# Optimization experiments

Hardware: AMD Instinct MI355X
Metric: run time of the kernel (lower is better)

## Reference

```python
import jax, jax.numpy as jnp
import numpy as np

B, LK, D, H = 16, 4096, 1024, 16
DK = D // H
EPS = 1e-5
NEG = -1.0e9


def _layernorm(x, g, b):
    m = jnp.mean(x, axis=-1, keepdims=True)
    v = jnp.mean((x - m) ** 2, axis=-1, keepdims=True)
    return (x - m) * jax.lax.rsqrt(v + EPS) * g + b


def setup_inputs() -> dict:
    key0 = jax.random.key(0)
    ks = jax.random.split(key0, 12)

    def lin(k, fan_in, fan_out):
        # torch nn.Linear default-ish scale; stored as [in, out] so y = x @ W + b
        return jax.random.normal(k, (fan_in, fan_out), jnp.float32) / np.float32(np.sqrt(fan_in))

    return {
        "query": jax.random.normal(ks[0], (B, 1, D), jnp.float32),
        "key": jax.random.normal(ks[1], (B, LK, D), jnp.float32),
        "mask": jax.random.randint(ks[2], (B, 1, LK), 0, 2, jnp.int32),
        "Wq": lin(ks[3], D, D), "bq": jnp.zeros((D,), jnp.float32),
        "Wk": lin(ks[4], D, D), "bk": jnp.zeros((D,), jnp.float32),
        "Wv": lin(ks[5], D, D), "bv": jnp.zeros((D,), jnp.float32),
        "Wo": lin(ks[6], D, D), "bo": jnp.zeros((D,), jnp.float32),
        "raw_thr": jnp.full((H, 1, 1), 0.1, jnp.float32),
        "Wvp": lin(ks[7], 2 * D, D),  # v_proj, no bias
        "W1": lin(ks[8], D, 2 * D), "b1": jnp.zeros((2 * D,), jnp.float32),
        "W2": lin(ks[9], 2 * D, D), "b2": jnp.zeros((D,), jnp.float32),
        "g1": jnp.ones((D,), jnp.float32), "be1": jnp.zeros((D,), jnp.float32),
        "g2": jnp.ones((D,), jnp.float32), "be2": jnp.zeros((D,), jnp.float32),
    }


def reference(query, key, mask, Wq, bq, Wk, bk, Wv, bv, Wo, bo, raw_thr,
              Wvp, W1, b1, W2, b2, g1, be1, g2, be2):
    b = query.shape[0]
    lk = key.shape[1]
    # v = cat(key, query.repeat(1, Lk, 1)) @ Wvp   (query has seq_len 1)
    v_in = jnp.concatenate([key, jnp.broadcast_to(query, (b, lk, D))], axis=2)
    v = v_in @ Wvp  # [B, Lk, D]

    Q = (query @ Wq + bq).reshape(b, 1, H, DK).transpose(0, 2, 1, 3)   # [B,H,1,DK]
    K = (key @ Wk + bk).reshape(b, lk, H, DK).transpose(0, 2, 1, 3)    # [B,H,Lk,DK]
    V = (v @ Wv + bv).reshape(b, lk, H, DK).transpose(0, 2, 1, 3)      # [B,H,Lk,DK]

    scores = jnp.einsum("bhqd,bhkd->bhqk", Q, K) / jnp.sqrt(jnp.float32(DK))
    # padding mask: [B,1,Lk] -> [B,1,1,Lk]
    scores = jnp.where(mask[:, None] == 0, NEG, scores)
    # learned per-head threshold: softplus(raw_thr) -> [1,H,1,1]
    thr = jax.nn.softplus(raw_thr)[None]
    scores = jnp.where(scores <= thr, NEG, scores)
    attn = jax.nn.softmax(scores, axis=-1)

    x = jnp.einsum("bhqk,bhkd->bhqd", attn, V)            # [B,H,1,DK]
    x = x.transpose(0, 2, 1, 3).reshape(b, 1, H * DK)      # [B,1,D]
    attn_out = x @ Wo + bo

    x = _layernorm(query + attn_out, g1, be1)
    ff = jax.nn.relu(x @ W1 + b1) @ W2 + b2
    x = _layernorm(x + ff, g2, be2)
    return x
```

## Files before the change

### kernel.cpp

```cpp
#include <hip/hip_runtime.h>
#include <hip/hip_bf16.h>

#define NB 16
#define NHD 16
#define ND 1024
#define NLK 4096
#define NFF 2048

typedef float f32x4 __attribute__((ext_vector_type(4)));
typedef float f32x2 __attribute__((ext_vector_type(2)));
typedef __bf16 bf16x2v __attribute__((ext_vector_type(2)));
typedef __bf16 bf16x4v __attribute__((ext_vector_type(4)));
typedef __bf16 bf16x8 __attribute__((ext_vector_type(8)));

__global__ void k_fill(float* out, int n, float v) {
  int i = blockIdx.x * 256 + threadIdx.x;
  if (i < n) out[i] = v;
}

__device__ __forceinline__ void gbar(unsigned* ctr, unsigned* flg, unsigned nblk) {
  __syncthreads();
  if (threadIdx.x == 0) {
    __hip_atomic_fetch_add(ctr, 1u, __ATOMIC_RELEASE, __HIP_MEMORY_SCOPE_AGENT);
    if (blockIdx.x == 0) {
      while (__hip_atomic_load(ctr, __ATOMIC_RELAXED, __HIP_MEMORY_SCOPE_AGENT) < nblk)
        __builtin_amdgcn_s_sleep(8);
      __hip_atomic_store(flg, 1u, __ATOMIC_RELEASE, __HIP_MEMORY_SCOPE_AGENT);
    } else {
      while (__hip_atomic_load(flg, __ATOMIC_RELAXED, __HIP_MEMORY_SCOPE_AGENT) == 0)
        __builtin_amdgcn_s_sleep(8);
    }
    __builtin_amdgcn_fence(__ATOMIC_ACQUIRE, "agent");
  }
  __syncthreads();
}

__global__ __launch_bounds__(256) void k_pre(const float* __restrict__ Wq,
                                             const float* __restrict__ bq,
                                             const float* __restrict__ Wvp,
                                             const float* __restrict__ query,
                                             const float* __restrict__ Wk,
                                             const float* __restrict__ bk,
                                             float* __restrict__ Qrow,
                                             float* __restrict__ cvec,
                                             __hip_bfloat16* __restrict__ wvpt,
                                             __hip_bfloat16* __restrict__ t_bf,
                                             float* __restrict__ s0,
                                             unsigned* __restrict__ bar) {
  __shared__ float pmem[9472];
  int blk = blockIdx.x;
  int t = threadIdx.x;
  if (blk < 128) {
    int which = blk >> 6;
    int jb = blk & 3;
    int i0 = ((blk >> 2) & 15) * 64;
    int j = jb * 256 + t;
    {
      int e = t * 4;
      int b = e >> 6, ii = e & 63;
      float4 v = *(const float4*)(query + (size_t)b * ND + i0 + ii);
      pmem[ii * 20 + b] = v.x;
      pmem[(ii + 1) * 20 + b] = v.y;
      pmem[(ii + 2) * 20 + b] = v.z;
      pmem[(ii + 3) * 20 + b] = v.w;
    }
    __syncthreads();
    float acc[16];
#pragma unroll
    for (int q = 0; q < 16; ++q) acc[q] = 0.f;
    for (int ii = 0; ii < 64; ++ii) {
      int i = i0 + ii;
      float wv = which ? Wvp[(size_t)(ND + i) * ND + j] : Wq[(size_t)i * ND + j];
      float qv[16];
      const float4* qp = (const float4*)&pmem[ii * 20];
      *(float4*)&qv[0] = qp[0];
      *(float4*)&qv[4] = qp[1];
      *(float4*)&qv[8] = qp[2];
      *(float4*)&qv[12] = qp[3];
#pragma unroll
      for (int q = 0; q < 16; ++q) acc[q] += wv * qv[q];
    }
    float* out = which ? cvec : Qrow;
    float bias = (!which && i0 == 0) ? bq[j] : 0.f;
#pragma unroll
    for (int q = 0; q < 16; ++q) atomicAdd(&out[q * ND + j], acc[q] + bias);
  } else {
    int tb = blk - 128;
    int n0 = (tb & 15) * 64;
    int k0base = (tb >> 4) * 256;
    for (int it = 0; it < 4; ++it) {
      int k0 = k0base + it * 64;
#pragma unroll
      for (int i = 0; i < 4; ++i) {
        int idx = t * 4 + i * 1024;
        int kk = idx >> 6, nn = idx & 63;
        float4 v = *(const float4*)(Wvp + (size_t)(k0 + kk) * ND + n0 + nn);
        pmem[kk * 68 + nn] = v.x;
        pmem[kk * 68 + nn + 1] = v.y;
        pmem[kk * 68 + nn + 2] = v.z;
        pmem[kk * 68 + nn + 3] = v.w;
      }
      __syncthreads();
#pragma unroll
      for (int i = 0; i < 4; ++i) {
        int idx = t * 4 + i * 1024;
        int nn = idx >> 6, kk = idx & 63;
        bf16x4v o;
#pragma unroll
        for (int j = 0; j < 4; ++j) o[j] = (__bf16)pmem[(kk + j) * 68 + nn];
        *(bf16x4v*)((__bf16*)wvpt + (size_t)(n0 + nn) * ND + k0 + kk) = o;
      }
      __syncthreads();
    }
  }
  gbar(&bar[5 * 32], &bar[256 + 5 * 32], 192);
  {
    int h = blk & 15, dblk = blk >> 4;
    float* qs = pmem;
    float* wks = pmem + 1024;
    if (blk < 128) {
      int lin = t * 4;
      int bb = lin >> 6, dk = lin & 63;
      *(float4*)&qs[bb * 64 + dk] = *(const float4*)(Qrow + bb * ND + h * 64 + dk);
#pragma unroll
      for (int e = 0; e < 8; ++e) {
        int l2 = e * 1024 + t * 4;
        int d = l2 >> 6, dk2 = l2 & 63;
        *(float4*)&wks[d * 66 + dk2] =
            *(const float4*)(Wk + (size_t)(dblk * 128 + d) * ND + h * 64 + dk2);
      }
    }
    __syncthreads();
    if (blk < 128) {
      if (dblk == 0 && t < 16) {
        float a = 0.f;
        const float* bkh = bk + h * 64;
        for (int jj = 0; jj < 64; ++jj) a += bkh[jj] * qs[t * 64 + jj];
        s0[t * 16 + h] = a;
      }
      int d = t >> 1, bh = (t & 1) * 8;
      float acc[8];
#pragma unroll
      for (int q = 0; q < 8; ++q) acc[q] = 0.f;
      for (int dk = 0; dk < 64; ++dk) {
        float wv = wks[d * 66 + dk];
#pragma unroll
        for (int q = 0; q < 8; ++q) acc[q] += wv * qs[(bh + q) * 64 + dk];
      }
#pragma unroll
      for (int q = 0; q < 8; ++q)
        t_bf[(size_t)((bh + q) * 16 + h) * ND + dblk * 128 + d] = (__hip_bfloat16)acc[q];
    }
  }
}

__global__ __launch_bounds__(512, 4) void k_flash(const float* __restrict__ key,
                                                  const __hip_bfloat16* __restrict__ t_bf,
                                                  const float* __restrict__ s0,
                                                  const float* __restrict__ raw_thr,
                                                  const int* __restrict__ mask,
                                                  __hip_bfloat16* __restrict__ pu,
                                                  float* __restrict__ mloc,
                                                  float* __restrict__ lloc) {
  int ch = blockIdx.x, b = blockIdx.y;
  int t = threadIdx.x;
  int wv = t >> 6, lane = t & 63, l15 = lane & 15, g4 = lane >> 4;
  __shared__ __align__(16) unsigned char lds_arena[79360];
  __bf16* kstage = (__bf16*)lds_arena;
  __bf16* psb = (__bf16*)(lds_arena + 65536);
  float* scr = (float*)(lds_arena + 74752);
  float* wls = (float*)(lds_arena + 76928);
  float* sm = (float*)(lds_arena + 78976);
  float* mrun = sm;
  float* lrun = sm + 16;
  float* fact = sm + 32;
  float* mnewv = sm + 48;
  float* thv = sm + 64;
  float* s0v = sm + 80;

  f32x2 pu_r[16];
#pragma unroll
  for (int h = 0; h < 16; ++h) pu_r[h] = (f32x2){0.f, 0.f};
  if (t < 16) {
    mrun[t] = -1.0e9f;
    lrun[t] = 0.f;
    thv[t] = log1pf(expf(raw_thr[t]));
    s0v[t] = s0[b * 16 + t];
  }
  __syncthreads();
  const float* keyb = key + (size_t)b * NLK * ND;
  const __hip_bfloat16* tb = t_bf + (size_t)(b * 16 + l15) * ND;
  int dsl = wv * 128;
  __bf16* kst_w = kstage + wv * 4096;
  int kk = t >> 4, hh = t & 15;
  int c16 = lane >> 2, bofs = (lane & 3) * 2;
  for (int sp = 0; sp < 4; ++sp) {
    int ks0 = ch * 128 + sp * 32;
    f32x4 sa0 = {0.f, 0.f, 0.f, 0.f}, sa1 = {0.f, 0.f, 0.f, 0.f};
#pragma unroll
    for (int st = 0; st < 4; ++st) {
      int d = dsl + st * 32 + g4 * 8;
      bf16x8 bfr = *(const bf16x8*)(tb + d);
      const float* a0p = keyb + (size_t)(ks0 + l15) * ND + d;
      const float* a1p = a0p + (size_t)16 * ND;
      float a0[8], a1[8];
      *(float4*)&a0[0] = *(const float4*)a0p;
      *(float4*)&a0[4] = *(const float4*)(a0p + 4);
      *(float4*)&a1[0] = *(const float4*)a1p;
      *(float4*)&a1[4] = *(const float4*)(a1p + 4);
      bf16x8 af0, af1;
#pragma unroll
      for (int j = 0; j < 8; ++j) {
        af0[j] = (__bf16)a0[j];
        af1[j] = (__bf16)a1[j];
      }
      int pos = (((st * 4 + g4) ^ l15) & 15) * 8;
      *(bf16x8*)(kst_w + l15 * 128 + pos) = af0;
      *(bf16x8*)(kst_w + (16 + l15) * 128 + pos) = af1;
      sa0 = __builtin_amdgcn_mfma_f32_16x16x32_bf16(af0, bfr, sa0, 0, 0, 0);
      sa1 = __builtin_amdgcn_mfma_f32_16x16x32_bf16(af1, bfr, sa1, 0, 0, 0);
    }
#pragma unroll
    for (int r = 0; r < 4; ++r) {
      psb[(wv * 32 + g4 * 4 + r) * 18 + l15] = (__bf16)sa0[r];
      psb[(wv * 32 + 16 + g4 * 4 + r) * 18 + l15] = (__bf16)sa1[r];
    }
    __syncthreads();
    float sum = 0.f;
#pragma unroll
    for (int w = 0; w < 8; ++w) sum += (float)psb[(w * 32 + kk) * 18 + hh];
    float sc_ = (sum + s0v[hh]) * 0.125f;
    int mv = mask[b * NLK + ks0 + kk];
    float sv = (mv != 0 && sc_ > thv[hh]) ? sc_ : -1.0e9f;
    scr[kk * 17 + hh] = sv;
    __syncthreads();
    if (wv == 0) {
      float m = -3.4e38f;
#pragma unroll
      for (int j = 0; j < 8; ++j) m = fmaxf(m, scr[(g4 * 8 + j) * 17 + l15]);
      m = fmaxf(m, __shfl_xor(m, 16, 64));
      m = fmaxf(m, __shfl_xor(m, 32, 64));
      if (lane < 16) {
        float mn = fmaxf(mrun[lane], m);
        mnewv[lane] = mn;
        fact[lane] = expf(mrun[lane] - mn);
        mrun[lane] = mn;
      }
    }
    __syncthreads();
    float w = expf(sv - mnewv[hh]);
    scr[kk * 17 + hh] = w;
    wls[kk * 16 + hh] = w;
    __syncthreads();
    if (wv == 0) {
      float s = 0.f;
#pragma unroll
      for (int j = 0; j < 8; ++j) s += scr[(g4 * 8 + j) * 17 + l15];
      s += __shfl_xor(s, 16, 64);
      s += __shfl_xor(s, 32, 64);
      if (lane < 16) lrun[lane] = lrun[lane] * fact[lane] + s;
    }
#pragma unroll
    for (int h = 0; h < 16; ++h) pu_r[h] *= fact[h];
    for (int k = 0; k < 32; ++k) {
      int phys = ((c16 ^ k) & 15) * 8;
      unsigned u = *(const unsigned*)(kst_w + k * 128 + phys + bofs);
      f32x2 kv;
      kv[0] = __uint_as_float(u << 16);
      kv[1] = __uint_as_float(u & 0xffff0000u);
      const f32x4* wr = (const f32x4*)&wls[k * 16];
      f32x4 w0 = wr[0], w1 = wr[1], w2 = wr[2], w3 = wr[3];
#pragma unroll
      for (int q = 0; q < 4; ++q) {
        pu_r[q] += w0[q] * kv;
        pu_r[4 + q] += w1[q] * kv;
        pu_r[8 + q] += w2[q] * kv;
        pu_r[12 + q] += w3[q] * kv;
      }
    }
  }
  int dlane = dsl + lane * 2;
  size_t pubase = (size_t)((b * 32 + ch) * 16) * ND + dlane;
#pragma unroll
  for (int h = 0; h < 16; ++h) {
    bf16x2v o;
    o[0] = (__bf16)pu_r[h][0];
    o[1] = (__bf16)pu_r[h][1];
    *(bf16x2v*)((__bf16*)pu + pubase + (size_t)h * ND) = o;
  }
  if (t < 16) {
    mloc[(b * 32 + ch) * 16 + t] = mrun[t];
    lloc[(b * 32 + ch) * 16 + t] = lrun[t];
  }
}

__global__ __launch_bounds__(256, 2) void k_tail(
    const __hip_bfloat16* __restrict__ pu, const float* __restrict__ mloc,
    const float* __restrict__ lloc, __hip_bfloat16* __restrict__ u_bf,
    const __hip_bfloat16* __restrict__ wvpt,
    const float* __restrict__ cvec, const float* __restrict__ Wv,
    const float* __restrict__ bv, float* __restrict__ attn_x,
    const float* __restrict__ Wo, const float* __restrict__ bo,
    const float* __restrict__ query, float* __restrict__ r1,
    const float* __restrict__ g1, const float* __restrict__ be1,
    const float* __restrict__ W1, float* __restrict__ h1,
    const float* __restrict__ b1, const float* __restrict__ W2,
    float* __restrict__ out2, const float* __restrict__ b2,
    const float* __restrict__ g2, const float* __restrict__ be2,
    float* __restrict__ outp, unsigned* __restrict__ bar) {
  __shared__ float smf[2176];
  int blk = blockIdx.x, t = threadIdx.x;
  int wv = t >> 6, lane = t & 63, l15 = lane & 15, g4 = lane >> 4;

  {
    int g = blk * 256 + t;
    if (g < 16384) {
      attn_x[g] = 0.f;
      r1[g] = 0.f;
      out2[g] = 0.f;
    }
    if (g < 32768) h1[g] = 0.f;
    int b = blk >> 4, h = blk & 15;
    if (t < 32) {
      float m = mloc[(b * 32 + t) * 16 + h];
      float l = lloc[(b * 32 + t) * 16 + h];
      float mg = m;
      for (int o = 16; o > 0; o >>= 1) mg = fmaxf(mg, __shfl_xor(mg, o, 32));
      float term = l * expf(m - mg);
      float ls = term;
      for (int o = 16; o > 0; o >>= 1) ls += __shfl_xor(ls, o, 32);
      smf[t] = expf(m - mg) / ls;
    }
    __syncthreads();
    int d = t * 4;
    f32x4 acc = {0.f, 0.f, 0.f, 0.f};
    for (int c = 0; c < 32; ++c) {
      bf16x4v v4 = *(const bf16x4v*)((const __bf16*)pu +
                                     (size_t)((b * 32 + c) * 16 + h) * ND + d);
      f32x4 v = {(float)v4[0], (float)v4[1], (float)v4[2], (float)v4[3]};
      acc += smf[c] * v;
    }
    bf16x4v o;
#pragma unroll
    for (int j = 0; j < 4; ++j) o[j] = (__bf16)acc[j];
    *(bf16x4v*)((__bf16*)u_bf + (size_t)(b * 16 + h) * ND + d) = o;
  }
  gbar(&bar[0 * 32], &bar[256 + 0 * 32], 256);

  {
    int h = blk >> 4, d0 = (blk & 15) * 64;
    float* vb = smf;
    const __hip_bfloat16* ub = u_bf + (size_t)(l15 * 16 + h) * ND;
    const __hip_bfloat16* wb = wvpt + (size_t)(d0 + wv * 16 + l15) * ND;
    f32x4 acc = {0.f, 0.f, 0.f, 0.f};
    for (int ks = 0; ks < 32; ++ks) {
      int d = ks * 32 + g4 * 8;
      bf16x8 a = *(const bf16x8*)(ub + d);
      bf16x8 bb = *(const bf16x8*)(wb + d);
      acc = __builtin_amdgcn_mfma_f32_16x16x32_bf16(a, bb, acc, 0, 0, 0);
    }
#pragma unroll
    for (int r = 0; r < 4; ++r) {
      int b = g4 * 4 + r;
      int nn = wv * 16 + l15;
      vb[b * 68 + nn] = acc[r] + cvec[(size_t)b * ND + d0 + nn];
    }
    __syncthreads();
    int joff = t & 63, bg = t >> 6;
    int j = h * 64 + joff;
    float ax[4] = {0.f, 0.f, 0.f, 0.f};
    for (int dd = 0; dd < 64; ++dd) {
      float wv_ = Wv[(size_t)(d0 + dd) * ND + j];
#pragma unroll
      for (int q = 0; q < 4; ++q) ax[q] += wv_ * vb[(bg * 4 + q) * 68 + dd];
    }
#pragma unroll
    for (int q = 0; q < 4; ++q) {
      float val = ax[q];
      if ((blk & 15) == 0) val += bv[j];
      atomicAdd(&attn_x[(size_t)(bg * 4 + q) * ND + j], val);
    }
  }
  gbar(&bar[1 * 32], &bar[256 + 1 * 32], 256);

  {
    int j0 = (blk & 7) * 128;
    int dc = blk >> 3;
    int d0 = dc * 32;
    float* ax = smf;
    if (t < 128) {
      int lin = t * 4;
      int bb = lin >> 5, dd = lin & 31;
      *(float4*)&ax[bb * 36 + dd] = *(const float4*)(attn_x + (size_t)bb * ND + d0 + dd);
    }
    __syncthreads();
    int joff = t & 127, bg = t >> 7;
    int j = j0 + joff;
    float acc[8];
#pragma unroll
    for (int q = 0; q < 8; ++q) acc[q] = 0.f;
    for (int dd = 0; dd < 32; ++dd) {
      float wv_ = Wo[(size_t)(d0 + dd) * ND + j];
#pragma unroll
      for (int q = 0; q < 8; ++q) acc[q] += wv_ * ax[(bg * 8 + q) * 36 + dd];
    }
#pragma unroll
    for (int q = 0; q < 8; ++q) {
      int bb = bg * 8 + q;
      float val = acc[q];
      if (dc == 0) val += bo[j] + query[(size_t)bb * ND + j];
      atomicAdd(&r1[(size_t)bb * ND + j], val);
    }
  }
  gbar(&bar[2 * 32], &bar[256 + 2 * 32], 256);

  {
    int n = (blk & 7) * 256 + t;
    int d0 = (blk >> 3) * 32;
    float* xs = smf;
    float* mv_s = smf + 1984;
    float* iv_s = smf + 2000;
    {
      int row = t >> 4, seg = t & 15;
      float s = 0.f, s2 = 0.f;
      const float* rp = r1 + (size_t)row * ND + seg * 64;
      for (int q = 0; q < 16; ++q) {
        float4 v = *(const float4*)(rp + q * 4);
        s += v.x + v.y + v.z + v.w;
        s2 += v.x * v.x + v.y * v.y + v.z * v.z + v.w * v.w;
      }
      for (int o = 1; o < 16; o <<= 1) {
        s += __shfl_xor(s, o, 16);
        s2 += __shfl_xor(s2, o, 16);
      }
      if (seg == 0) {
        float mean = s * (1.f / ND);
        float var = s2 * (1.f / ND) - mean * mean;
        mv_s[row] = mean;
        iv_s[row] = rsqrtf(var + 1e-5f);
      }
    }
    __syncthreads();
    if (t < 128) {
      int e = t * 4;
      int bb = e >> 5, dd = e & 31;
      float4 v = *(const float4*)(r1 + (size_t)bb * ND + d0 + dd);
      float4 g = *(const float4*)(g1 + d0 + dd);
      float4 be = *(const float4*)(be1 + d0 + dd);
      float m = mv_s[bb], iv = iv_s[bb];
      xs[bb * 36 + dd] = (v.x - m) * iv * g.x + be.x;
      xs[bb * 36 + dd + 1] = (v.y - m) * iv * g.y + be.y;
      xs[bb * 36 + dd + 2] = (v.z - m) * iv * g.z + be.z;
      xs[bb * 36 + dd + 3] = (v.w - m) * iv * g.w + be.w;
    }
    __syncthreads();
    float acc[16];
#pragma unroll
    for (int q = 0; q < 16; ++q) acc[q] = 0.f;
    for (int dd = 0; dd < 32; ++dd) {
      float wv_ = W1[(size_t)(d0 + dd) * NFF + n];
#pragma unroll
      for (int q = 0; q < 16; ++q) acc[q] += wv_ * xs[q * 36 + dd];
    }
#pragma unroll
    for (int q = 0; q < 16; ++q) atomicAdd(&h1[(size_t)q * NFF + n], acc[q]);
  }
  gbar(&bar[3 * 32], &bar[256 + 3 * 32], 256);

  {
    int j0 = (blk & 7) * 128;
    int n0 = (blk >> 3) * 64;
    float* hs = smf;
    {
      int lin = t * 4;
      int bb = lin >> 6, nn = lin & 63;
      float4 hv = *(const float4*)(h1 + (size_t)bb * NFF + n0 + nn);
      float4 bb1 = *(const float4*)(b1 + n0 + nn);
      hs[bb * 68 + nn] = fmaxf(hv.x + bb1.x, 0.f);
      hs[bb * 68 + nn + 1] = fmaxf(hv.y + bb1.y, 0.f);
      hs[bb * 68 + nn + 2] = fmaxf(hv.z + bb1.z, 0.f);
      hs[bb * 68 + nn + 3] = fmaxf(hv.w + bb1.w, 0.f);
    }
    __syncthreads();
    int joff = t & 127, bg = t >> 7;
    int j = j0 + joff;
    float acc[8];
#pragma unroll
    for (int q = 0; q < 8; ++q) acc[q] = 0.f;
    for (int nn = 0; nn < 64; ++nn) {
      float wv_ = W2[(size_t)(n0 + nn) * ND + j];
#pragma unroll
      for (int q = 0; q < 8; ++q) acc[q] += wv_ * hs[(bg * 8 + q) * 68 + nn];
    }
#pragma unroll
    for (int q = 0; q < 8; ++q) atomicAdd(&out2[(size_t)(bg * 8 + q) * ND + j], acc[q]);
  }
  gbar(&bar[4 * 32], &bar[256 + 4 * 32], 256);

  if (blk < 16) {
    int b = blk;
    float* rs = smf;
    float* rs2 = smf + 256;
    float4 v = *(const float4*)(r1 + (size_t)b * ND + t * 4);
    float s = v.x + v.y + v.z + v.w;
    float s2 = v.x * v.x + v.y * v.y + v.z * v.z + v.w * v.w;
    rs[t] = s;
    rs2[t] = s2;
    __syncthreads();
    for (int st = 128; st > 0; st >>= 1) {
      if (t < st) {
        rs[t] += rs[t + st];
        rs2[t] += rs2[t + st];
      }
      __syncthreads();
    }
    float mean = rs[0] * (1.f / ND);
    float var = rs2[0] * (1.f / ND) - mean * mean;
    float inv = rsqrtf(var + 1e-5f);
    float4 g = *(const float4*)(g1 + t * 4);
    float4 be = *(const float4*)(be1 + t * 4);
    float4 o2 = *(const float4*)(out2 + (size_t)b * ND + t * 4);
    float4 bb2 = *(const float4*)(b2 + t * 4);
    float4 v2;
    v2.x = (v.x - mean) * inv * g.x + be.x + o2.x + bb2.x;
    v2.y = (v.y - mean) * inv * g.y + be.y + o2.y + bb2.y;
    v2.z = (v.z - mean) * inv * g.z + be.z + o2.z + bb2.z;
    v2.w = (v.w - mean) * inv * g.w + be.w + o2.w + bb2.w;
    __syncthreads();
    s = v2.x + v2.y + v2.z + v2.w;
    s2 = v2.x * v2.x + v2.y * v2.y + v2.z * v2.z + v2.w * v2.w;
    rs[t] = s;
    rs2[t] = s2;
    __syncthreads();
    for (int st = 128; st > 0; st >>= 1) {
      if (t < st) {
        rs[t] += rs[t + st];
        rs2[t] += rs2[t + st];
      }
      __syncthreads();
    }
    float mean2 = rs[0] * (1.f / ND);
    float var2 = rs2[0] * (1.f / ND) - mean2 * mean2;
    float inv2 = rsqrtf(var2 + 1e-5f);
    float4 gg = *(const float4*)(g2 + t * 4);
    float4 bbe = *(const float4*)(be2 + t * 4);
    float4 o;
    o.x = (v2.x - mean2) * inv2 * gg.x + bbe.x;
    o.y = (v2.y - mean2) * inv2 * gg.y + bbe.y;
    o.z = (v2.z - mean2) * inv2 * gg.z + bbe.z;
    o.w = (v2.w - mean2) * inv2 * gg.w + bbe.w;
    *(float4*)(outp + (size_t)b * ND + t * 4) = o;
  }
}

extern "C" void kernel_launch(void* const* d_in, const int* in_sizes, int n_in,
                              void* d_out, int out_size, void* d_ws, size_t ws_size,
                              hipStream_t stream) {
  const float* query = (const float*)d_in[0];
  const float* key = (const float*)d_in[1];
  const int* mask = (const int*)d_in[2];
  const float* Wq = (const float*)d_in[3];
  const float* bq = (const float*)d_in[4];
  const float* Wk = (const float*)d_in[5];
  const float* bk = (const float*)d_in[6];
  const float* Wv = (const float*)d_in[7];
  const float* bv = (const float*)d_in[8];
  const float* Wo = (const float*)d_in[9];
  const float* bo = (const float*)d_in[10];
  const float* raw_thr = (const float*)d_in[11];
  const float* Wvp = (const float*)d_in[12];
  const float* W1 = (const float*)d_in[13];
  const float* b1 = (const float*)d_in[14];
  const float* W2 = (const float*)d_in[15];
  const float* b2 = (const float*)d_in[16];
  const float* g1 = (const float*)d_in[17];
  const float* be1 = (const float*)d_in[18];
  const float* g2 = (const float*)d_in[19];
  const float* be2 = (const float*)d_in[20];

  const size_t OFF_QROW = 0;
  const size_t OFF_C = 65536;
  const size_t OFF_BAR = 131072;
  const size_t ZERO_BYTES = 135168;
  const size_t OFF_ATTNX = 135168;
  const size_t OFF_R1 = 200704;
  const size_t OFF_H1 = 266240;
  const size_t OFF_OUT2 = 397312;
  const size_t OFF_S0 = 462848;
  const size_t OFF_MLOC = 463872;
  const size_t OFF_LLOC = 496640;
  const size_t OFF_TBF = 529408;
  const size_t OFF_UBF = 1053696;
  const size_t OFF_WVPT = 1577984;
  const size_t OFF_PU = 4723712;
  const size_t TOTAL = 21500928;

  if (ws_size < TOTAL) {
    k_fill<<<dim3((out_size + 255) / 256), dim3(256), 0, stream>>>((float*)d_out, out_size,
                                                                   12345.0f);
    return;
  }

  char* wsb = (char*)d_ws;
  float* Qrow = (float*)(wsb + OFF_QROW);
  float* cvec = (float*)(wsb + OFF_C);
  unsigned* bar = (unsigned*)(wsb + OFF_BAR);
  float* attn_x = (float*)(wsb + OFF_ATTNX);
  float* r1 = (float*)(wsb + OFF_R1);
  float* h1 = (float*)(wsb + OFF_H1);
  float* out2 = (float*)(wsb + OFF_OUT2);
  float* s0 = (float*)(wsb + OFF_S0);
  float* mloc = (float*)(wsb + OFF_MLOC);
  float* lloc = (float*)(wsb + OFF_LLOC);
  __hip_bfloat16* t_bf = (__hip_bfloat16*)(wsb + OFF_TBF);
  __hip_bfloat16* u_bf = (__hip_bfloat16*)(wsb + OFF_UBF);
  __hip_bfloat16* wvpt = (__hip_bfloat16*)(wsb + OFF_WVPT);
  __hip_bfloat16* pu = (__hip_bfloat16*)(wsb + OFF_PU);

  hipMemsetAsync(d_ws, 0, ZERO_BYTES, stream);

  k_pre<<<dim3(192), dim3(256), 0, stream>>>(Wq, bq, Wvp, query, Wk, bk, Qrow, cvec, wvpt,
                                             t_bf, s0, bar);
  k_flash<<<dim3(32, 16), dim3(512), 0, stream>>>(key, t_bf, s0, raw_thr, mask, pu, mloc, lloc);
  k_tail<<<dim3(256), dim3(256), 0, stream>>>(pu, mloc, lloc, u_bf, wvpt, cvec, Wv, bv,
                                              attn_x, Wo, bo, query, r1, g1, be1, W1, h1, b1,
                                              W2, out2, b2, g2, be2, (float*)d_out, bar);
}
```

Before: 192.3 us.

## Fuse prologue kernel into flash kernel using grid-wide barriers

Merges the k_pre prologue (Q/cvec projections, Wvp transpose, t_bf precompute) into the k_flash kernel as a 512-block persistent launch separated by two software grid barriers. The prologue work is repartitioned for 512-thread blocks. The aim is to drop one kernel launch and the inter-kernel gap. In exchange, all 512 blocks must be co-resident for the barriers to work, and most blocks sit idle through the prologue phases. The barrier flag offsets in k_tail are shifted to match the new layout.

```diff
diff --git a/kernel.cpp b/kernel.cpp
--- a/kernel.cpp
+++ b/kernel.cpp
@@ -35,262 +35,258 @@
   __syncthreads();
 }
 
-__global__ __launch_bounds__(256) void k_pre(const float* __restrict__ Wq,
-                                             const float* __restrict__ bq,
-                                             const float* __restrict__ Wvp,
-                                             const float* __restrict__ query,
-                                             const float* __restrict__ Wk,
-                                             const float* __restrict__ bk,
-                                             float* __restrict__ Qrow,
-                                             float* __restrict__ cvec,
-                                             __hip_bfloat16* __restrict__ wvpt,
-                                             __hip_bfloat16* __restrict__ t_bf,
-                                             float* __restrict__ s0,
-                                             unsigned* __restrict__ bar) {
-  __shared__ float pmem[9472];
-  int blk = blockIdx.x;
-  int t = threadIdx.x;
+__global__ __launch_bounds__(512, 4) void k_flash(
+    const float* __restrict__ Wq, const float* __restrict__ bq,
+    const float* __restrict__ Wvp, const float* __restrict__ query,
+    const float* __restrict__ Wk, const float* __restrict__ bk,
+    float* __restrict__ Qrow, float* __restrict__ cvec,
+    __hip_bfloat16* __restrict__ wvpt, __hip_bfloat16* __restrict__ t_bf,
+    float* __restrict__ s0,
+    const float* __restrict__ key, const float* __restrict__ raw_thr,
+    const int* __restrict__ mask, __hip_bfloat16* __restrict__ pu,
+    float* __restrict__ mloc, float* __restrict__ lloc,
+    unsigned* __restrict__ bar) {
+  __shared__ __align__(16) unsigned char lds_arena[79360];
+  float* af = (float*)lds_arena;
+  int blk = blockIdx.x, t = threadIdx.x;
+  int wv = t >> 6, lane = t & 63, l15 = lane & 15, g4 = lane >> 4;
+  int half = t >> 8, vt = t & 255;
+
   if (blk < 128) {
     int which = blk >> 6;
-    int jb = blk & 3;
-    int i0 = ((blk >> 2) & 15) * 64;
-    int j = jb * 256 + t;
-    {
+    int jb = (blk >> 5) & 1;
+    int i0c = blk & 31;
+    int i0 = i0c * 32;
+    int j = jb * 512 + t;
+    if (t < 128) {
       int e = t * 4;
-      int b = e >> 6, ii = e & 63;
+      int b = e >> 5, ii = e & 31;
       float4 v = *(const float4*)(query + (size_t)b * ND + i0 + ii);
-      pmem[ii * 20 + b] = v.x;
-      pmem[(ii + 1) * 20 + b] = v.y;
-      pmem[(ii + 2) * 20 + b] = v.z;
-      pmem[(ii + 3) * 20 + b] = v.w;
+      af[ii * 20 + b] = v.x;
+      af[(ii + 1) * 20 + b] = v.y;
+      af[(ii + 2) * 20 + b] = v.z;
+      af[(ii + 3) * 20 + b] = v.w;
     }
     __syncthreads();
     float acc[16];
 #pragma unroll
     for (int q = 0; q < 16; ++q) acc[q] = 0.f;
-    for (int ii = 0; ii < 64; ++ii) {
+    for (int ii = 0; ii < 32; ++ii) {
       int i = i0 + ii;
-      float wv = which ? Wvp[(size_t)(ND + i) * ND + j] : Wq[(size_t)i * ND + j];
+      float wvv = which ? Wvp[(size_t)(ND + i) * ND + j] : Wq[(size_t)i * ND + j];
       float qv[16];
-      const float4* qp = (const float4*)&pmem[ii * 20];
+      const float4* qp = (const float4*)&af[ii * 20];
       *(float4*)&qv[0] = qp[0];
       *(float4*)&qv[4] = qp[1];
       *(float4*)&qv[8] = qp[2];
       *(float4*)&qv[12] = qp[3];
 #pragma unroll
-      for (int q = 0; q < 16; ++q) acc[q] += wv * qv[q];
+      for (int q = 0; q < 16; ++q) acc[q] += wvv * qv[q];
     }
     float* out = which ? cvec : Qrow;
-    float bias = (!which && i0 == 0) ? bq[j] : 0.f;
+    float bias = (!which && i0c == 0) ? bq[j] : 0.f;
 #pragma unroll
     for (int q = 0; q < 16; ++q) atomicAdd(&out[q * ND + j], acc[q] + bias);
-  } else {
+  } else if (blk < 192) {
     int tb = blk - 128;
     int n0 = (tb & 15) * 64;
     int k0base = (tb >> 4) * 256;
     for (int it = 0; it < 4; ++it) {
       int k0 = k0base + it * 64;
 #pragma unroll
-      for (int i = 0; i < 4; ++i) {
-        int idx = t * 4 + i * 1024;
+      for (int i = 0; i < 2; ++i) {
+        int idx = t * 4 + i * 2048;
         int kk = idx >> 6, nn = idx & 63;
         float4 v = *(const float4*)(Wvp + (size_t)(k0 + kk) * ND + n0 + nn);
-        pmem[kk * 68 + nn] = v.x;
-        pmem[kk * 68 + nn + 1] = v.y;
-        pmem[kk * 68 + nn + 2] = v.z;
-        pmem[kk * 68 + nn + 3] = v.w;
-      }
-      __syncthreads();
-#pragma unroll
-      for (int i = 0; i < 4; ++i) {
-        int idx = t * 4 + i * 1024;
+        af[kk * 68 + nn] = v.x;
+        af[kk * 68 + nn + 1] = v.y;
+        af[kk * 68 + nn + 2] = v.z;
+        af[kk * 68 + nn + 3] = v.w;
+      }
+      __syncthreads();
+#pragma unroll
+      for (int i = 0; i < 2; ++i) {
+        int idx = t * 4 + i * 2048;
         int nn = idx >> 6, kk = idx & 63;
         bf16x4v o;
 #pragma unroll
-        for (int j = 0; j < 4; ++j) o[j] = (__bf16)pmem[(kk + j) * 68 + nn];
+        for (int jj = 0; jj < 4; ++jj) o[jj] = (__bf16)af[(kk + jj) * 68 + nn];
         *(bf16x4v*)((__bf16*)wvpt + (size_t)(n0 + nn) * ND + k0 + kk) = o;
       }
       __syncthreads();
     }
   }
-  gbar(&bar[5 * 32], &bar[256 + 5 * 32], 192);
-  {
-    int h = blk & 15, dblk = blk >> 4;
-    float* qs = pmem;
-    float* wks = pmem + 1024;
-    if (blk < 128) {
-      int lin = t * 4;
+  gbar(&bar[6 * 32], &bar[512 + 6 * 32], 512);
+
+  if (blk < 64) {
+    int h = blk & 15;
+    int dblk = (blk >> 4) * 2 + half;
+    float* pm = af + half * 9472;
+    float* qs = pm;
+    float* wks = pm + 1024;
+    {
+      int lin = vt * 4;
       int bb = lin >> 6, dk = lin & 63;
       *(float4*)&qs[bb * 64 + dk] = *(const float4*)(Qrow + bb * ND + h * 64 + dk);
-#pragma unroll
-      for (int e = 0; e < 8; ++e) {
-        int l2 = e * 1024 + t * 4;
-        int d = l2 >> 6, dk2 = l2 & 63;
-        *(float4*)&wks[d * 66 + dk2] =
-            *(const float4*)(Wk + (size_t)(dblk * 128 + d) * ND + h * 64 + dk2);
-      }
-    }
-    __syncthreads();
-    if (blk < 128) {
-      if (dblk == 0 && t < 16) {
-        float a = 0.f;
-        const float* bkh = bk + h * 64;
-        for (int jj = 0; jj < 64; ++jj) a += bkh[jj] * qs[t * 64 + jj];
-        s0[t * 16 + h] = a;
-      }
-      int d = t >> 1, bh = (t & 1) * 8;
-      float acc[8];
-#pragma unroll
-      for (int q = 0; q < 8; ++q) acc[q] = 0.f;
-      for (int dk = 0; dk < 64; ++dk) {
-        float wv = wks[d * 66 + dk];
-#pragma unroll
-        for (int q = 0; q < 8; ++q) acc[q] += wv * qs[(bh + q) * 64 + dk];
-      }
-#pragma unroll
-      for (int q = 0; q < 8; ++q)
-        t_bf[(size_t)((bh + q) * 16 + h) * ND + dblk * 128 + d] = (__hip_bfloat16)acc[q];
-    }
-  }
-}
-
-__global__ __launch_bounds__(512, 4) void k_flash(const float* __restrict__ key,
-                                                  const __hip_bfloat16* __restrict__ t_bf,
-                                                  const float* __restrict__ s0,
-                                                  const float* __restrict__ raw_thr,
-                                                  const int* __restrict__ mask,
-                                                  __hip_bfloat16* __restrict__ pu,
-                                                  float* __restrict__ mloc,
-                                                  float* __restrict__ lloc) {
-  int ch = blockIdx.x, b = blockIdx.y;
-  int t = threadIdx.x;
-  int wv = t >> 6, lane = t & 63, l15 = lane & 15, g4 = lane >> 4;
-  __shared__ __align__(16) unsigned char lds_arena[79360];
-  __bf16* kstage = (__bf16*)lds_arena;
-  __bf16* psb = (__bf16*)(lds_arena + 65536);
-  float* scr = (float*)(lds_arena + 74752);
-  float* wls = (float*)(lds_arena + 76928);
-  float* sm = (float*)(lds_arena + 78976);
-  float* mrun = sm;
-  float* lrun = sm + 16;
-  float* fact = sm + 32;
-  float* mnewv = sm + 48;
-  float* thv = sm + 64;
-  float* s0v = sm + 80;
-
-  f32x2 pu_r[16];
-#pragma unroll
-  for (int h = 0; h < 16; ++h) pu_r[h] = (f32x2){0.f, 0.f};
-  if (t < 16) {
-    mrun[t] = -1.0e9f;
-    lrun[t] = 0.f;
-    thv[t] = log1pf(expf(raw_thr[t]));
-    s0v[t] = s0[b * 16 + t];
-  }
-  __syncthreads();
-  const float* keyb = key + (size_t)b * NLK * ND;
-  const __hip_bfloat16* tb = t_bf + (size_t)(b * 16 + l15) * ND;
-  int dsl = wv * 128;
-  __bf16* kst_w = kstage + wv * 4096;
-  int kk = t >> 4, hh = t & 15;
-  int c16 = lane >> 2, bofs = (lane & 3) * 2;
-  for (int sp = 0; sp < 4; ++sp) {
-    int ks0 = ch * 128 + sp * 32;
-    f32x4 sa0 = {0.f, 0.f, 0.f, 0.f}, sa1 = {0.f, 0.f, 0.f, 0.f};
-#pragma unroll
-    for (int st = 0; st < 4; ++st) {
-      int d = dsl + st * 32 + g4 * 8;
-      bf16x8 bfr = *(const bf16x8*)(tb + d);
-      const float* a0p = keyb + (size_t)(ks0 + l15) * ND + d;
-      const float* a1p = a0p + (size_t)16 * ND;
-      float a0[8], a1[8];
-      *(float4*)&a0[0] = *(const float4*)a0p;
-      *(float4*)&a0[4] = *(const float4*)(a0p + 4);
-      *(float4*)&a1[0] = *(const float4*)a1p;
-      *(float4*)&a1[4] = *(const float4*)(a1p + 4);
-      bf16x8 af0, af1;
-#pragma unroll
-      for (int j = 0; j < 8; ++j) {
-        af0[j] = (__bf16)a0[j];
-        af1[j] = (__bf16)a1[j];
-      }
-      int pos = (((st * 4 + g4) ^ l15) & 15) * 8;
-      *(bf16x8*)(kst_w + l15 * 128 + pos) = af0;
-      *(bf16x8*)(kst_w + (16 + l15) * 128 + pos) = af1;
-      sa0 = __builtin_amdgcn_mfma_f32_16x16x32_bf16(af0, bfr, sa0, 0, 0, 0);
-      sa1 = __builtin_amdgcn_mfma_f32_16x16x32_bf16(af1, bfr, sa1, 0, 0, 0);
-    }
-#pragma unroll
-    for (int r = 0; r < 4; ++r) {
-      psb[(wv * 32 + g4 * 4 + r) * 18 + l15] = (__bf16)sa0[r];
-      psb[(wv * 32 + 16 + g4 * 4 + r) * 18 + l15] = (__bf16)sa1[r];
-    }
-    __syncthreads();
-    float sum = 0.f;
-#pragma unroll
-    for (int w = 0; w < 8; ++w) sum += (float)psb[(w * 32 + kk) * 18 + hh];
-    float sc_ = (sum + s0v[hh]) * 0.125f;
-    int mv = mask[b * NLK + ks0 + kk];
-    float sv = (mv != 0 && sc_ > thv[hh]) ? sc_ : -1.0e9f;
-    scr[kk * 17 + hh] = sv;
-    __syncthreads();
-    if (wv == 0) {
-      float m = -3.4e38f;
-#pragma unroll
-      for (int j = 0; j < 8; ++j) m = fmaxf(m, scr[(g4 * 8 + j) * 17 + l15]);
-      m = fmaxf(m, __shfl_xor(m, 16, 64));
-      m = fmaxf(m, __shfl_xor(m, 32, 64));
-      if (lane < 16) {
-        float mn = fmaxf(mrun[lane], m);
-        mnewv[lane] = mn;
-        fact[lane] = expf(mrun[lane] - mn);
-        mrun[lane] = mn;
-      }
-    }
-    __syncthreads();
-    float w = expf(sv - mnewv[hh]);
-    scr[kk * 17 + hh] = w;
-    wls[kk * 16 + hh] = w;
-    __syncthreads();
-    if (wv == 0) {
-      float s = 0.f;
-#pragma unroll
-      for (int j = 0; j < 8; ++j) s += scr[(g4 * 8 + j) * 17 + l15];
-      s += __shfl_xor(s, 16, 64);
-      s += __shfl_xor(s, 32, 64);
-      if (lane < 16) lrun[lane] = lrun[lane] * fact[lane] + s;
-    }
-#pragma unroll
-    for (int h = 0; h < 16; ++h) pu_r[h] *= fact[h];
-    for (int k = 0; k < 32; ++k) {
-      int phys = ((c16 ^ k) & 15) * 8;
-      unsigned u = *(const unsigned*)(kst_w + k * 128 + phys + bofs);
-      f32x2 kv;
-      kv[0] = __uint_as_float(u << 16);
-      kv[1] = __uint_as_float(u & 0xffff0000u);
-      const f32x4* wr = (const f32x4*)&wls[k * 16];
-      f32x4 w0 = wr[0], w1 = wr[1], w2 = wr[2], w3 = wr[3];
-#pragma unroll
-      for (int q = 0; q < 4; ++q) {
-        pu_r[q] += w0[q] * kv;
-        pu_r[4 + q] += w1[q] * kv;
-        pu_r[8 + q] += w2[q] * kv;
-        pu_r[12 + q] += w3[q] * kv;
-      }
-    }
-  }
-  int dlane = dsl + lane * 2;
-  size_t pubase = (size_t)((b * 32 + ch) * 16) * ND + dlane;
-#pragma unroll
-  for (int h = 0; h < 16; ++h) {
-    bf16x2v o;
-    o[0] = (__bf16)pu_r[h][0];
-    o[1] = (__bf16)pu_r[h][1];
-    *(bf16x2v*)((__bf16*)pu + pubase + (size_t)h * ND) = o;
-  }
-  if (t < 16) {
-    mloc[(b * 32 + ch) * 16 + t] = mrun[t];
-    lloc[(b * 32 + ch) * 16 + t] = lrun[t];
+    }
+#pragma unroll
+    for (int e = 0; e < 8; ++e) {
+      int l2 = e * 1024 + vt * 4;
+      int d = l2 >> 6, dk2 = l2 & 63;
+      *(float4*)&wks[d * 66 + dk2] =
+          *(const float4*)(Wk + (size_t)(dblk * 128 + d) * ND + h * 64 + dk2);
+    }
+    __syncthreads();
+    if (dblk == 0 && vt < 16) {
+      float a = 0.f;
+      const float* bkh = bk + h * 64;
+      for (int jj = 0; jj < 64; ++jj) a += bkh[jj] * qs[vt * 64 + jj];
+      s0[vt * 16 + h] = a;
+    }
+    int d = vt >> 1, bh = (vt & 1) * 8;
+    float acc[8];
+#pragma unroll
+    for (int q = 0; q < 8; ++q) acc[q] = 0.f;
+    for (int dk = 0; dk < 64; ++dk) {
+      float wvv = wks[d * 66 + dk];
+#pragma unroll
+      for (int q = 0; q < 8; ++q) acc[q] += wvv * qs[(bh + q) * 64 + dk];
+    }
+#pragma unroll
+    for (int q = 0; q < 8; ++q)
+      t_bf[(size_t)((bh + q) * 16 + h) * ND + dblk * 128 + d] = (__hip_bfloat16)acc[q];
+  }
+  gbar(&bar[7 * 32], &bar[512 + 7 * 32], 512);
+
+  {
+    int ch = blk & 31, b = blk >> 5;
+    __bf16* kstage = (__bf16*)lds_arena;
+    __bf16* psb = (__bf16*)(lds_arena + 65536);
+    float* scr = (float*)(lds_arena + 74752);
+    float* wls = (float*)(lds_arena + 76928);
+    float* sm = (float*)(lds_arena + 78976);
+    float* mrun = sm;
+    float* lrun = sm + 16;
+    float* fact = sm + 32;
+    float* mnewv = sm + 48;
+    float* thv = sm + 64;
+    float* s0v = sm + 80;
+
+    f32x2 pu_r[16];
+#pragma unroll
+    for (int h = 0; h < 16; ++h) pu_r[h] = (f32x2){0.f, 0.f};
+    __syncthreads();
+    if (t < 16) {
+      mrun[t] = -1.0e9f;
+      lrun[t] = 0.f;
+      thv[t] = log1pf(expf(raw_thr[t]));
+      s0v[t] = s0[b * 16 + t];
+    }
+    __syncthreads();
+    const float* keyb = key + (size_t)b * NLK * ND;
+    const __hip_bfloat16* tb = t_bf + (size_t)(b * 16 + l15) * ND;
+    int dsl = wv * 128;
+    __bf16* kst_w = kstage + wv * 4096;
+    int kk = t >> 4, hh = t & 15;
+    int c16 = lane >> 2, bofs = (lane & 3) * 2;
+    for (int sp = 0; sp < 4; ++sp) {
+      int ks0 = ch * 128 + sp * 32;
+      f32x4 sa0 = {0.f, 0.f, 0.f, 0.f}, sa1 = {0.f, 0.f, 0.f, 0.f};
+#pragma unroll
+      for (int st = 0; st < 4; ++st) {
+        int d = dsl + st * 32 + g4 * 8;
+        bf16x8 bfr = *(const bf16x8*)(tb + d);
+        const float* a0p = keyb + (size_t)(ks0 + l15) * ND + d;
+        const float* a1p = a0p + (size_t)16 * ND;
+        float a0[8], a1[8];
+        *(float4*)&a0[0] = *(const float4*)a0p;
+        *(float4*)&a0[4] = *(const float4*)(a0p + 4);
+        *(float4*)&a1[0] = *(const float4*)a1p;
+        *(float4*)&a1[4] = *(const float4*)(a1p + 4);
+        bf16x8 af0, af1;
+#pragma unroll
+        for (int j = 0; j < 8; ++j) {
+          af0[j] = (__bf16)a0[j];
+          af1[j] = (__bf16)a1[j];
+        }
+        int pos = (((st * 4 + g4) ^ l15) & 15) * 8;
+        *(bf16x8*)(kst_w + l15 * 128 + pos) = af0;
+        *(bf16x8*)(kst_w + (16 + l15) * 128 + pos) = af1;
+        sa0 = __builtin_amdgcn_mfma_f32_16x16x32_bf16(af0, bfr, sa0, 0, 0, 0);
+        sa1 = __builtin_amdgcn_mfma_f32_16x16x32_bf16(af1, bfr, sa1, 0, 0, 0);
+      }
+#pragma unroll
+      for (int r = 0; r < 4; ++r) {
+        psb[(wv * 32 + g4 * 4 + r) * 18 + l15] = (__bf16)sa0[r];
+        psb[(wv * 32 + 16 + g4 * 4 + r) * 18 + l15] = (__bf16)sa1[r];
+      }
+      __syncthreads();
+      float sum = 0.f;
+#pragma unroll
+      for (int w = 0; w < 8; ++w) sum += (float)psb[(w * 32 + kk) * 18 + hh];
+      float sc_ = (sum + s0v[hh]) * 0.125f;
+      int mv = mask[b * NLK + ks0 + kk];
+      float sv = (mv != 0 && sc_ > thv[hh]) ? sc_ : -1.0e9f;
+      scr[kk * 17 + hh] = sv;
+      __syncthreads();
+      if (wv == 0) {
+        float m = -3.4e38f;
+#pragma unroll
+        for (int j = 0; j < 8; ++j) m = fmaxf(m, scr[(g4 * 8 + j) * 17 + l15]);
+        m = fmaxf(m, __shfl_xor(m, 16, 64));
+        m = fmaxf(m, __shfl_xor(m, 32, 64));
+        if (lane < 16) {
+          float mn = fmaxf(mrun[lane], m);
+          mnewv[lane] = mn;
+          fact[lane] = expf(mrun[lane] - mn);
+          mrun[lane] = mn;
+        }
+      }
+      __syncthreads();
+      float w = expf(sv - mnewv[hh]);
+      scr[kk * 17 + hh] = w;
+      wls[kk * 16 + hh] = w;
+      __syncthreads();
+      if (wv == 0) {
+        float s = 0.f;
+#pragma unroll
+        for (int j = 0; j < 8; ++j) s += scr[(g4 * 8 + j) * 17 + l15];
+        s += __shfl_xor(s, 16, 64);
+        s += __shfl_xor(s, 32, 64);
+        if (lane < 16) lrun[lane] = lrun[lane] * fact[lane] + s;
+      }
+#pragma unroll
+      for (int h = 0; h < 16; ++h) pu_r[h] *= fact[h];
+      for (int k = 0; k < 32; ++k) {
+        int phys = ((c16 ^ k) & 15) * 8;
+        unsigned u = *(const unsigned*)(kst_w + k * 128 + phys + bofs);
+        f32x2 kv;
+        kv[0] = __uint_as_float(u << 16);
+        kv[1] = __uint_as_float(u & 0xffff0000u);
+        const f32x4* wr = (const f32x4*)&wls[k * 16];
+        f32x4 w0 = wr[0], w1 = wr[1], w2 = wr[2], w3 = wr[3];
+#pragma unroll
+        for (int q = 0; q < 4; ++q) {
+          pu_r[q] += w0[q] * kv;
+          pu_r[4 + q] += w1[q] * kv;
+          pu_r[8 + q] += w2[q] * kv;
+          pu_r[12 + q] += w3[q] * kv;
+        }
+      }
+    }
+    int dlane = dsl + lane * 2;
+    size_t pubase = (size_t)((b * 32 + ch) * 16) * ND + dlane;
+#pragma unroll
+    for (int h = 0; h < 16; ++h) {
+      bf16x2v o;
+      o[0] = (__bf16)pu_r[h][0];
+      o[1] = (__bf16)pu_r[h][1];
+      *(bf16x2v*)((__bf16*)pu + pubase + (size_t)h * ND) = o;
+    }
+    if (t < 16) {
+      mloc[(b * 32 + ch) * 16 + t] = mrun[t];
+      lloc[(b * 32 + ch) * 16 + t] = lrun[t];
+    }
   }
 }
 
@@ -345,7 +341,7 @@
     for (int j = 0; j < 4; ++j) o[j] = (__bf16)acc[j];
     *(bf16x4v*)((__bf16*)u_bf + (size_t)(b * 16 + h) * ND + d) = o;
   }
-  gbar(&bar[0 * 32], &bar[256 + 0 * 32], 256);
+  gbar(&bar[0 * 32], &bar[512 + 0 * 32], 256);
 
   {
     int h = blk >> 4, d0 = (blk & 15) * 64;
@@ -381,7 +377,7 @@
       atomicAdd(&attn_x[(size_t)(bg * 4 + q) * ND + j], val);
     }
   }
-  gbar(&bar[1 * 32], &bar[256 + 1 * 32], 256);
+  gbar(&bar[1 * 32], &bar[512 + 1 * 32], 256);
 
   {
     int j0 = (blk & 7) * 128;
@@ -412,7 +408,7 @@
       atomicAdd(&r1[(size_t)bb * ND + j], val);
     }
   }
-  gbar(&bar[2 * 32], &bar[256 + 2 * 32], 256);
+  gbar(&bar[2 * 32], &bar[512 + 2 * 32], 256);
 
   {
     int n = (blk & 7) * 256 + t;
@@ -465,7 +461,7 @@
 #pragma unroll
     for (int q = 0; q < 16; ++q) atomicAdd(&h1[(size_t)q * NFF + n], acc[q]);
   }
-  gbar(&bar[3 * 32], &bar[256 + 3 * 32], 256);
+  gbar(&bar[3 * 32], &bar[512 + 3 * 32], 256);
 
   {
     int j0 = (blk & 7) * 128;
@@ -495,7 +491,7 @@
 #pragma unroll
     for (int q = 0; q < 8; ++q) atomicAdd(&out2[(size_t)(bg * 8 + q) * ND + j], acc[q]);
   }
-  gbar(&bar[4 * 32], &bar[256 + 4 * 32], 256);
+  gbar(&bar[4 * 32], &bar[512 + 4 * 32], 256);
 
   if (blk < 16) {
     int b = blk;
@@ -619,9 +615,9 @@
 
   hipMemsetAsync(d_ws, 0, ZERO_BYTES, stream);
 
-  k_pre<<<dim3(192), dim3(256), 0, stream>>>(Wq, bq, Wvp, query, Wk, bk, Qrow, cvec, wvpt,
-                                             t_bf, s0, bar);
-  k_flash<<<dim3(32, 16), dim3(512), 0, stream>>>(key, t_bf, s0, raw_thr, mask, pu, mloc, lloc);
+  k_flash<<<dim3(512), dim3(512), 0, stream>>>(Wq, bq, Wvp, query, Wk, bk, Qrow, cvec, wvpt,
+                                               t_bf, s0, key, raw_thr, mask, pu, mloc, lloc,
+                                               bar);
   k_tail<<<dim3(256), dim3(256), 0, stream>>>(pu, mloc, lloc, u_bf, wvpt, cvec, Wv, bv,
                                               attn_x, Wo, bo, query, r1, g1, be1, W1, h1, b1,
                                               W2, out2, b2, g2, be2, (float*)d_out, bar);
```

After: 289.7 us. 50.6% more time.
